# Kernel optimization log

Measured on AMD Instinct MI355X. Metric: run time of the kernel, lower is better.

Reference implementation:

```python
import jax, jax.numpy as jnp
import numpy as np

K = 8
TERMS = 6


def setup_inputs() -> dict:
    key = jax.random.key(0)
    k1, k2 = jax.random.split(key)
    b, s, d = 4, 512, 512
    x = jax.random.normal(k1, (b, s, d), dtype=jnp.float32)
    # scale connection so lie_element entries are O(1) and the 6-term Taylor
    # series is a sane approximation of exp (d_model=512 sum would otherwise blow up)
    A = jax.random.normal(k2, (b, s, d, K, K), dtype=jnp.float32) * (1.0 / d)
    return {"x": x, "A": A}


def reference(x, A):
    # lie_element[b,i,j,k,l] = sum_d (x[b,i,d] - x[b,j,d]) * A[b,j,d,k,l]
    # computed WITHOUT materializing the [b,s,s,d,k,k] broadcast intermediate.
    lie_i = jnp.einsum('bid,bjdkl->bijkl', x, A)   # x_i term
    lie_j = jnp.einsum('bjd,bjdkl->bjkl', x, A)    # x_j term (diagonal in j)
    M = -(lie_i - lie_j[:, None, :, :, :])          # [b,s,s,k,k]
    k = M.shape[-1]
    I = jnp.eye(k, dtype=M.dtype)
    result = jnp.broadcast_to(I, M.shape)
    M_power = result
    for n in range(1, TERMS + 1):
        M_power = jnp.matmul(M_power, M) / n
        result = result + M_power
    return result
```

## Files before the change

kernel.cpp:

```cpp
#include <hip/hip_runtime.h>


typedef short short8 __attribute__((ext_vector_type(8)));
typedef float f32x4 __attribute__((ext_vector_type(4)));

constexpr int S = 512, D = 512, MM = 64;
constexpr int TILE_I = 128;
constexpr int TS_STRIDE = 65;
constexpr int RES_STRIDE = 68;

__device__ inline unsigned pack2(float lo, float hi) {
  unsigned a = __float_as_uint(lo) + 0x8000u;
  unsigned b = __float_as_uint(hi) + 0x8000u;
  return __builtin_amdgcn_perm(b, a, 0x07060302);
}

__global__ __launch_bounds__(256, 3)
void pt_kernel(const float* __restrict__ x, const float* __restrict__ A,
               float* __restrict__ out) {
  const int bid = blockIdx.x;
  const int b = bid >> 11;
  const int j = (bid >> 2) & (S - 1);
  const int i0 = (bid & 3) * TILE_I;
  const int t = threadIdx.x;
  const int w = t >> 6;
  const int L = t & 63;
  const int quad = L >> 4;
  const int l15 = L & 15;

  __shared__ short8 Bf[8 * 64];
  __shared__ float TsRes[TILE_I * RES_STRIDE];
  __shared__ float Tjrow[MM];
  __shared__ float red[4][MM];

  const float* xb = x + (size_t)b * S * D;
  const float* Ab = A + (size_t)(b * S + j) * (size_t)(D * MM);

  {
    const int m = t & 63;
    const int part = t >> 6;
    const float* xj = xb + (size_t)j * D;
    const int dbeg = part * (D / 4);
    float acc = 0.f;
    for (int dd = 0; dd < D / 4; ++dd)
      acc += xj[dbeg + dd] * Ab[(size_t)(dbeg + dd) * MM + m];
    red[part][m] = acc;
  }
  __syncthreads();
  if (t < MM) Tjrow[t] = red[0][t] + red[1][t] + red[2][t] + red[3][t];

  f32x4 acc[2][4];
#pragma unroll
  for (int it = 0; it < 2; ++it)
#pragma unroll
    for (int mt = 0; mt < 4; ++mt) acc[it][mt] = (f32x4){0.f, 0.f, 0.f, 0.f};

  const int mcol = w * 16 + l15;
  const float* xrow0 = xb + (size_t)(i0 + w * 32 + l15) * D;
  const float* xrow1 = xrow0 + (size_t)16 * D;

  for (int d0 = 0; d0 < D; d0 += 64) {
    __syncthreads();
#pragma unroll
    for (int kk = 0; kk < 2; ++kk) {
      const float* ap = Ab + (size_t)(d0 + kk * 32 + quad * 8) * MM + mcol;
      const float e0 = ap[0 * MM], e1 = ap[1 * MM], e2 = ap[2 * MM], e3 = ap[3 * MM];
      const float e4 = ap[4 * MM], e5 = ap[5 * MM], e6 = ap[6 * MM], e7 = ap[7 * MM];
      union { unsigned u[4]; short8 s; } bf;
      bf.u[0] = pack2(e0, e1); bf.u[1] = pack2(e2, e3);
      bf.u[2] = pack2(e4, e5); bf.u[3] = pack2(e6, e7);
      Bf[(kk * 4 + w) * 64 + L] = bf.s;
    }
    __syncthreads();
#pragma unroll
    for (int kk = 0; kk < 2; ++kk) {
      short8 bfr[4];
#pragma unroll
      for (int mt = 0; mt < 4; ++mt) bfr[mt] = Bf[(kk * 4 + mt) * 64 + L];
#pragma unroll
      for (int it = 0; it < 2; ++it) {
        const float* xp = (it ? xrow1 : xrow0) + d0 + kk * 32 + quad * 8;
        const float4 v0 = *(const float4*)xp;
        const float4 v1 = *(const float4*)(xp + 4);
        union { unsigned u[4]; short8 s; } af;
        af.u[0] = pack2(v0.x, v0.y); af.u[1] = pack2(v0.z, v0.w);
        af.u[2] = pack2(v1.x, v1.y); af.u[3] = pack2(v1.z, v1.w);
#pragma unroll
        for (int mt = 0; mt < 4; ++mt)
          acc[it][mt] = __builtin_amdgcn_mfma_f32_16x16x32_bf16(af.s, bfr[mt], acc[it][mt], 0, 0, 0);
      }
    }
  }

#pragma unroll
  for (int it = 0; it < 2; ++it)
#pragma unroll
    for (int mt = 0; mt < 4; ++mt)
#pragma unroll
      for (int r = 0; r < 4; ++r)
        TsRes[(w * 32 + it * 16 + quad * 4 + r) * TS_STRIDE + mt * 16 + l15] = acc[it][mt][r];
  __syncthreads();

  {
    const int i_loc = t >> 1;
    const int r0 = (t & 1) * 4;

    float Mi[8][8];
#pragma unroll
    for (int k = 0; k < 8; ++k)
#pragma unroll
      for (int l = 0; l < 8; ++l)
        Mi[k][l] = Tjrow[k * 8 + l] - TsRes[i_loc * TS_STRIDE + k * 8 + l];
    __syncthreads();

    float Mp[4][8], res[4][8];
#pragma unroll
    for (int r = 0; r < 4; ++r)
#pragma unroll
      for (int c = 0; c < 8; ++c) {
        const float v = Mi[r0 + r][c];
        Mp[r][c] = v;
        res[r][c] = v + ((r0 + r) == c ? 1.0f : 0.0f);
      }

    const float invn[5] = {0.5f, 1.0f / 3.0f, 0.25f, 0.2f, 1.0f / 6.0f};
#pragma unroll
    for (int n = 0; n < 5; ++n) {
      float np[4][8];
#pragma unroll
      for (int r = 0; r < 4; ++r)
#pragma unroll
        for (int c = 0; c < 8; ++c) {
          float sum = 0.f;
#pragma unroll
          for (int k = 0; k < 8; ++k) sum += Mp[r][k] * Mi[k][c];
          np[r][c] = sum * invn[n];
        }
#pragma unroll
      for (int r = 0; r < 4; ++r)
#pragma unroll
        for (int c = 0; c < 8; ++c) {
          Mp[r][c] = np[r][c];
          res[r][c] += np[r][c];
        }
    }

#pragma unroll
    for (int r = 0; r < 4; ++r) {
      *(float4*)&TsRes[i_loc * RES_STRIDE + (r0 + r) * 8] =
          make_float4(res[r][0], res[r][1], res[r][2], res[r][3]);
      *(float4*)&TsRes[i_loc * RES_STRIDE + (r0 + r) * 8 + 4] =
          make_float4(res[r][4], res[r][5], res[r][6], res[r][7]);
    }
  }
  __syncthreads();

  {
    const int part = t & 15;
    const int il0 = t >> 4;
#pragma unroll
    for (int step = 0; step < 8; ++step) {
      const int i_loc = il0 + step * 16;
      const int i = i0 + i_loc;
      const float4 v = *(const float4*)&TsRes[i_loc * RES_STRIDE + part * 4];
      *(float4*)(out + (((size_t)(b * S + i)) * S + j) * MM + part * 4) = v;
    }
  }
}

extern "C" void kernel_launch(void* const* d_in, const int* in_sizes, int n_in,
                              void* d_out, int out_size, void* d_ws, size_t ws_size,
                              hipStream_t stream) {
  const float* x = (const float*)d_in[0];
  const float* A = (const float*)d_in[1];
  float* out = (float*)d_out;
  const int B = in_sizes[0] / (S * D);
  pt_kernel<<<dim3(B * S * 4), dim3(256), 0, stream>>>(x, A, out);
}
```

Baseline: 868.0 us.

## Fold x_j difference into MFMA input, halve LDS tile, raise occupancy

Removes the separate x_j·A reduction by computing (x_j - x_i) before bf16 packing, so a single MFMA produces M directly. The epilogue is split into two halves so the shared result tile shrinks to 64 rows, and launch bounds are raised to 6 blocks per CU to allow higher occupancy. Blocks are remapped with an interleaving swizzle and output uses nontemporal stores. Tighter register limits may cause spills, and packing the difference changes bf16 rounding slightly.

```diff
diff --git a/kernel.cpp b/kernel.cpp
--- a/kernel.cpp
+++ b/kernel.cpp
@@ -15,13 +15,15 @@
   return __builtin_amdgcn_perm(b, a, 0x07060302);
 }
 
-__global__ __launch_bounds__(256, 3)
+__global__ __launch_bounds__(256, 6)
 void pt_kernel(const float* __restrict__ x, const float* __restrict__ A,
                float* __restrict__ out) {
   const int bid = blockIdx.x;
-  const int b = bid >> 11;
-  const int j = (bid >> 2) & (S - 1);
-  const int i0 = (bid & 3) * TILE_I;
+  const int q = gridDim.x >> 3;
+  const int work = (bid & 7) * q + (bid >> 3);
+  const int b = work >> 11;
+  const int j = (work >> 2) & (S - 1);
+  const int i0 = (work & 3) * TILE_I;
   const int t = threadIdx.x;
   const int w = t >> 6;
   const int L = t & 63;
@@ -29,25 +31,11 @@
   const int l15 = L & 15;
 
   __shared__ short8 Bf[8 * 64];
-  __shared__ float TsRes[TILE_I * RES_STRIDE];
-  __shared__ float Tjrow[MM];
-  __shared__ float red[4][MM];
+  __shared__ float TsRes[64 * RES_STRIDE];
 
   const float* xb = x + (size_t)b * S * D;
   const float* Ab = A + (size_t)(b * S + j) * (size_t)(D * MM);
-
-  {
-    const int m = t & 63;
-    const int part = t >> 6;
-    const float* xj = xb + (size_t)j * D;
-    const int dbeg = part * (D / 4);
-    float acc = 0.f;
-    for (int dd = 0; dd < D / 4; ++dd)
-      acc += xj[dbeg + dd] * Ab[(size_t)(dbeg + dd) * MM + m];
-    red[part][m] = acc;
-  }
-  __syncthreads();
-  if (t < MM) Tjrow[t] = red[0][t] + red[1][t] + red[2][t] + red[3][t];
+  const float* xjr = xb + (size_t)j * D;
 
   f32x4 acc[2][4];
 #pragma unroll
@@ -77,14 +65,19 @@
       short8 bfr[4];
 #pragma unroll
       for (int mt = 0; mt < 4; ++mt) bfr[mt] = Bf[(kk * 4 + mt) * 64 + L];
+      const float* xjp = xjr + d0 + kk * 32 + quad * 8;
+      const float4 j0 = *(const float4*)xjp;
+      const float4 j1 = *(const float4*)(xjp + 4);
 #pragma unroll
       for (int it = 0; it < 2; ++it) {
         const float* xp = (it ? xrow1 : xrow0) + d0 + kk * 32 + quad * 8;
         const float4 v0 = *(const float4*)xp;
         const float4 v1 = *(const float4*)(xp + 4);
         union { unsigned u[4]; short8 s; } af;
-        af.u[0] = pack2(v0.x, v0.y); af.u[1] = pack2(v0.z, v0.w);
-        af.u[2] = pack2(v1.x, v1.y); af.u[3] = pack2(v1.z, v1.w);
+        af.u[0] = pack2(j0.x - v0.x, j0.y - v0.y);
+        af.u[1] = pack2(j0.z - v0.z, j0.w - v0.w);
+        af.u[2] = pack2(j1.x - v1.x, j1.y - v1.y);
+        af.u[3] = pack2(j1.z - v1.z, j1.w - v1.w);
 #pragma unroll
         for (int mt = 0; mt < 4; ++mt)
           acc[it][mt] = __builtin_amdgcn_mfma_f32_16x16x32_bf16(af.s, bfr[mt], acc[it][mt], 0, 0, 0);
@@ -93,77 +86,80 @@
   }
 
 #pragma unroll
-  for (int it = 0; it < 2; ++it)
+  for (int h = 0; h < 2; ++h) {
+    if (h) __syncthreads();
 #pragma unroll
     for (int mt = 0; mt < 4; ++mt)
 #pragma unroll
       for (int r = 0; r < 4; ++r)
-        TsRes[(w * 32 + it * 16 + quad * 4 + r) * TS_STRIDE + mt * 16 + l15] = acc[it][mt][r];
-  __syncthreads();
-
-  {
-    const int i_loc = t >> 1;
-    const int r0 = (t & 1) * 4;
-
-    float Mi[8][8];
-#pragma unroll
-    for (int k = 0; k < 8; ++k)
-#pragma unroll
-      for (int l = 0; l < 8; ++l)
-        Mi[k][l] = Tjrow[k * 8 + l] - TsRes[i_loc * TS_STRIDE + k * 8 + l];
+        TsRes[(w * 16 + quad * 4 + r) * TS_STRIDE + mt * 16 + l15] = acc[h][mt][r];
     __syncthreads();
 
-    float Mp[4][8], res[4][8];
+    {
+      const int i_loc = t >> 2;
+      const int r0 = (t & 3) * 2;
+
+      float Mi[8][8];
 #pragma unroll
-    for (int r = 0; r < 4; ++r)
+      for (int k = 0; k < 8; ++k)
 #pragma unroll
-      for (int c = 0; c < 8; ++c) {
-        const float v = Mi[r0 + r][c];
-        Mp[r][c] = v;
-        res[r][c] = v + ((r0 + r) == c ? 1.0f : 0.0f);
+        for (int l = 0; l < 8; ++l)
+          Mi[k][l] = TsRes[i_loc * TS_STRIDE + k * 8 + l];
+      __syncthreads();
+
+      float Mp[2][8], res[2][8];
+#pragma unroll
+      for (int r = 0; r < 2; ++r)
+#pragma unroll
+        for (int c = 0; c < 8; ++c) {
+          const float v = Mi[r0 + r][c];
+          Mp[r][c] = v;
+          res[r][c] = v + ((r0 + r) == c ? 1.0f : 0.0f);
+        }
+
+      const float invn[5] = {0.5f, 1.0f / 3.0f, 0.25f, 0.2f, 1.0f / 6.0f};
+#pragma unroll
+      for (int n = 0; n < 5; ++n) {
+        float np[2][8];
+#pragma unroll
+        for (int r = 0; r < 2; ++r)
+#pragma unroll
+          for (int c = 0; c < 8; ++c) {
+            float sum = 0.f;
+#pragma unroll
+            for (int k = 0; k < 8; ++k) sum += Mp[r][k] * Mi[k][c];
+            np[r][c] = sum * invn[n];
+          }
+#pragma unroll
+        for (int r = 0; r < 2; ++r)
+#pragma unroll
+          for (int c = 0; c < 8; ++c) {
+            Mp[r][c] = np[r][c];
+            res[r][c] += np[r][c];
+          }
       }
 
-    const float invn[5] = {0.5f, 1.0f / 3.0f, 0.25f, 0.2f, 1.0f / 6.0f};
 #pragma unroll
-    for (int n = 0; n < 5; ++n) {
-      float np[4][8];
+      for (int r = 0; r < 2; ++r) {
+        f32x4 lo = {res[r][0], res[r][1], res[r][2], res[r][3]};
+        f32x4 hi = {res[r][4], res[r][5], res[r][6], res[r][7]};
+        *(f32x4*)&TsRes[i_loc * RES_STRIDE + (r0 + r) * 8] = lo;
+        *(f32x4*)&TsRes[i_loc * RES_STRIDE + (r0 + r) * 8 + 4] = hi;
+      }
+    }
+    __syncthreads();
+
+    {
+      const int part = t & 15;
+      const int il = t >> 4;
 #pragma unroll
-      for (int r = 0; r < 4; ++r)
-#pragma unroll
-        for (int c = 0; c < 8; ++c) {
-          float sum = 0.f;
-#pragma unroll
-          for (int k = 0; k < 8; ++k) sum += Mp[r][k] * Mi[k][c];
-          np[r][c] = sum * invn[n];
-        }
-#pragma unroll
-      for (int r = 0; r < 4; ++r)
-#pragma unroll
-        for (int c = 0; c < 8; ++c) {
-          Mp[r][c] = np[r][c];
-          res[r][c] += np[r][c];
-        }
-    }
-
-#pragma unroll
-    for (int r = 0; r < 4; ++r) {
-      *(float4*)&TsRes[i_loc * RES_STRIDE + (r0 + r) * 8] =
-          make_float4(res[r][0], res[r][1], res[r][2], res[r][3]);
-      *(float4*)&TsRes[i_loc * RES_STRIDE + (r0 + r) * 8 + 4] =
-          make_float4(res[r][4], res[r][5], res[r][6], res[r][7]);
-    }
-  }
-  __syncthreads();
-
-  {
-    const int part = t & 15;
-    const int il0 = t >> 4;
-#pragma unroll
-    for (int step = 0; step < 8; ++step) {
-      const int i_loc = il0 + step * 16;
-      const int i = i0 + i_loc;
-      const float4 v = *(const float4*)&TsRes[i_loc * RES_STRIDE + part * 4];
-      *(float4*)(out + (((size_t)(b * S + i)) * S + j) * MM + part * 4) = v;
+      for (int step = 0; step < 4; ++step) {
+        const int iL = step * 16 + il;
+        const int i = i0 + step * 32 + h * 16 + il;
+        const f32x4 v = *(const f32x4*)&TsRes[iL * RES_STRIDE + part * 4];
+        __builtin_nontemporal_store(v,
+            (f32x4*)(out + (((size_t)(b * S + i)) * S + j) * MM + part * 4));
+      }
     }
   }
 }
```

After: 1.943 ms. 2.24x slower.
